# Optimization experiments

Measured on AMD Instinct MI355X. Metric: run time of the kernel, lower is better.

## Reference

```python
import jax, jax.numpy as jnp
import numpy as np

B, N, CIN = 4, 8192, 256
H, D = 8, 64            # n_heads, head_n_channels
INNER = H * D           # 512
COUT = 256
EPS = 1e-5              # torch InstanceNorm1d default eps


def setup_inputs() -> dict:
    key = jax.random.key(0)
    ks = jax.random.split(key, 8)
    s = 1.0 / np.sqrt(CIN)
    return {
        "u_x": jax.random.normal(ks[0], (B, N, CIN), dtype=jnp.float32),
        "pos_x": jax.random.uniform(ks[1], (B, N, 2), dtype=jnp.float32),
        # torch nn.Linear weights have shape (out_features, in_features)
        "Wq": jax.random.normal(ks[2], (INNER, CIN), dtype=jnp.float32) * s,
        "Wk": jax.random.normal(ks[3], (INNER, CIN), dtype=jnp.float32) * s,
        "Wv": jax.random.normal(ks[4], (INNER, CIN), dtype=jnp.float32) * s,
        "Wo": jax.random.normal(ks[5], (COUT, INNER), dtype=jnp.float32) * (1.0 / np.sqrt(INNER)),
        "bo": jax.random.normal(ks[6], (COUT,), dtype=jnp.float32) * 0.01,
    }


def _heads(x, W):
    # x: [B,N,CIN] @ W.T -> [B,N,H*D] -> [B,H,N,D]
    y = jnp.einsum("bnc,ec->bne", x, W)
    return y.reshape(x.shape[0], x.shape[1], H, D).transpose(0, 2, 1, 3)


def _inorm(u):
    # Matches torch: InstanceNorm1d applied to (B*H, N, D) normalizes over the
    # LAST dim (D) per (batch, head, grid point), biased variance, no affine.
    mean = jnp.mean(u, axis=-1, keepdims=True)
    var = jnp.mean(jnp.square(u - mean), axis=-1, keepdims=True)
    return (u - mean) / jnp.sqrt(var + EPS)


def reference(u_x, pos_x, Wq, Wk, Wv, Wo, bo):
    batch, n = u_x.shape[0], u_x.shape[1]
    q = _heads(u_x, Wq)          # [B,H,N,D]
    k = _inorm(_heads(u_x, Wk))  # u_y = u_x (self-attention path)
    v = _inorm(_heads(u_x, Wv))
    # associative path: (K^T V) then Q; uniform weights = 1/N
    dots = jnp.einsum("bhnd,bhne->bhde", k, v)   # [B,H,D,D]
    u = jnp.einsum("bhnd,bhde->bhne", q, dots) / n
    u = u.transpose(0, 2, 1, 3).reshape(batch, n, INNER)
    return jnp.einsum("bne,oe->bno", u, Wo) + bo
```

## Files before the change

kernel.cpp:

```cpp
#include <hip/hip_runtime.h>


#define B_    4
#define N_    8192
#define CIN_  256
#define H_    8
#define D_    64
#define INNER_ 512
#define COUT_ 256
#define EPS_  1e-5f

typedef unsigned short ushort_t;
typedef unsigned int   uint_t;
typedef __attribute__((ext_vector_type(8))) short short8;
typedef __attribute__((ext_vector_type(4))) float f32x4;

__device__ __forceinline__ void split_bf16(float x, ushort_t& hi, ushort_t& lo) {
  const uint_t u = __float_as_uint(x);
  const uint_t hr = (u + 0x8000u) & 0xffff0000u;
  hi = (ushort_t)(hr >> 16);
  const float l = x - __uint_as_float(hr);
  lo = (ushort_t)((__float_as_uint(l) + 0x8000u) >> 16);
}

__device__ __forceinline__ void cvt8(float4 x, float4 y, uint4& uh, uint4& ul) {
  const float v[8] = {x.x, x.y, x.z, x.w, y.x, y.y, y.z, y.w};
  ushort_t h[8], l[8];
#pragma unroll
  for (int j = 0; j < 8; j++) split_bf16(v[j], h[j], l[j]);
  uh = make_uint4(h[0] | ((uint_t)h[1] << 16), h[2] | ((uint_t)h[3] << 16),
                  h[4] | ((uint_t)h[5] << 16), h[6] | ((uint_t)h[7] << 16));
  ul = make_uint4(l[0] | ((uint_t)l[1] << 16), l[2] | ((uint_t)l[3] << 16),
                  l[4] | ((uint_t)l[5] << 16), l[6] | ((uint_t)l[7] << 16));
}

#define MFMA(A, Bv, C) __builtin_amdgcn_mfma_f32_16x16x32_bf16((A), (Bv), (C), 0, 0, 0)

__global__ __launch_bounds__(256) void prep_all_kernel(
    const float* __restrict__ u_x, const float* __restrict__ Wk,
    const float* __restrict__ Wv, ushort_t* __restrict__ uxH,
    ushort_t* __restrict__ uxL, ushort_t* __restrict__ WkvH,
    ushort_t* __restrict__ WkvL, float* __restrict__ dots)
{
  const int bid = blockIdx.x;
  if (bid < 4096) {
    const size_t base = ((size_t)bid * 256 + threadIdx.x) * 8;
    const float4 x = *(const float4*)(u_x + base);
    const float4 y = *(const float4*)(u_x + base + 4);
    uint4 uh, ul;
    cvt8(x, y, uh, ul);
    *(uint4*)(uxH + base) = uh;
    *(uint4*)(uxL + base) = ul;
  } else {
    const int wb = bid - 4096;
    const size_t base = ((size_t)wb * 256 + threadIdx.x) * 8;
    const float* src = (base < 131072) ? (Wk + base) : (Wv + base - 131072);
    const float4 x = *(const float4*)(src);
    const float4 y = *(const float4*)(src + 4);
    uint4 uh, ul;
    cvt8(x, y, uh, ul);
    *(uint4*)(WkvH + base) = uh;
    *(uint4*)(WkvL + base) = ul;
    *(float4*)(dots + ((size_t)wb * 256 + threadIdx.x) * 4) =
        make_float4(0.f, 0.f, 0.f, 0.f);
  }
}

__global__ __launch_bounds__(256, 2) void kv_dots_kernel(
    const ushort_t* __restrict__ uxH, const ushort_t* __restrict__ uxL,
    const ushort_t* __restrict__ WkvH, const ushort_t* __restrict__ WkvL,
    float* __restrict__ dots)
{
  __shared__ __align__(16) char smem[66560];
  ushort_t* KtH = (ushort_t*)(smem);
  ushort_t* KtL = (ushort_t*)(smem + 9216);
  ushort_t* VtH = (ushort_t*)(smem + 18432);
  ushort_t* VtL = (ushort_t*)(smem + 27648);

  const int t = threadIdx.x;
  const int chunk = blockIdx.x, h = blockIdx.y, b = blockIdx.z;
  const int lane = t & 63, wave = t >> 6;
  const int q = lane >> 4, r = lane & 15;
  const int m0 = (wave >> 1) * 64, n0 = (wave & 1) * 64;
  const int srow = t >> 1, scs = (t & 1) * 16, q0 = (t & 1) * 2;
  const int dstripe = 16 * wave;

  const int wr = (srow < 64) ? (h * 64 + srow) : (512 + h * 64 + srow - 64);
  const ushort_t* bgH = WkvH + (size_t)wr * CIN_ + scs;
  const ushort_t* bgL = WkvL + (size_t)wr * CIN_ + scs;

  f32x4 dacc[4];
#pragma unroll
  for (int j = 0; j < 4; j++) dacc[j] = (f32x4)0.f;

  for (int mt = 0; mt < 2; mt++) {
    const int r0 = chunk * 256 + mt * 128;
    const ushort_t* agH = uxH + ((size_t)(b * N_) + r0 + srow) * CIN_ + scs;
    const ushort_t* agL = uxL + ((size_t)(b * N_) + r0 + srow) * CIN_ + scs;

    f32x4 acc[4][4];
#pragma unroll
    for (int i = 0; i < 4; i++)
#pragma unroll
      for (int j = 0; j < 4; j++) acc[i][j] = (f32x4)0.f;

    {
      const uint4 a0 = *(const uint4*)(agH);
      const uint4 a1 = *(const uint4*)(agH + 8);
      const uint4 l0 = *(const uint4*)(agL);
      const uint4 l1 = *(const uint4*)(agL + 8);
      const uint4 b0 = *(const uint4*)(bgH);
      const uint4 b1 = *(const uint4*)(bgH + 8);
      const uint4 c0 = *(const uint4*)(bgL);
      const uint4 c1 = *(const uint4*)(bgL + 8);
      ushort_t (*Ah)[130][8] = (ushort_t(*)[130][8])(smem);
      ushort_t (*Al)[130][8] = (ushort_t(*)[130][8])(smem + 8320);
      ushort_t (*Bh)[130][8] = (ushort_t(*)[130][8])(smem + 16640);
      ushort_t (*Bl)[130][8] = (ushort_t(*)[130][8])(smem + 24960);
      *(uint4*)&Ah[q0][srow][0] = a0;  *(uint4*)&Ah[q0 + 1][srow][0] = a1;
      *(uint4*)&Al[q0][srow][0] = l0;  *(uint4*)&Al[q0 + 1][srow][0] = l1;
      *(uint4*)&Bh[q0][srow][0] = b0;  *(uint4*)&Bh[q0 + 1][srow][0] = b1;
      *(uint4*)&Bl[q0][srow][0] = c0;  *(uint4*)&Bl[q0 + 1][srow][0] = c1;
    }
    __syncthreads();

#pragma unroll 2
    for (int kc = 0; kc < 8; kc++) {
      const int cur = kc & 1, nxt = cur ^ 1;
      uint4 a0, a1, l0, l1, b0, b1, c0, c1;
      if (kc < 7) {
        const int off = (kc + 1) * 32;
        a0 = *(const uint4*)(agH + off);  a1 = *(const uint4*)(agH + off + 8);
        l0 = *(const uint4*)(agL + off);  l1 = *(const uint4*)(agL + off + 8);
        b0 = *(const uint4*)(bgH + off);  b1 = *(const uint4*)(bgH + off + 8);
        c0 = *(const uint4*)(bgL + off);  c1 = *(const uint4*)(bgL + off + 8);
      }
      char* sc = smem + cur * 33280;
      ushort_t (*Ah)[130][8] = (ushort_t(*)[130][8])(sc);
      ushort_t (*Al)[130][8] = (ushort_t(*)[130][8])(sc + 8320);
      ushort_t (*Bh)[130][8] = (ushort_t(*)[130][8])(sc + 16640);
      ushort_t (*Bl)[130][8] = (ushort_t(*)[130][8])(sc + 24960);
      short8 ahf[4], alf[4];
#pragma unroll
      for (int mi = 0; mi < 4; mi++) {
        ahf[mi] = *(const short8*)&Ah[q][m0 + 16 * mi + r][0];
        alf[mi] = *(const short8*)&Al[q][m0 + 16 * mi + r][0];
      }
#pragma unroll
      for (int nj = 0; nj < 4; nj++) {
        const short8 bhv = *(const short8*)&Bh[q][n0 + 16 * nj + r][0];
        const short8 blv = *(const short8*)&Bl[q][n0 + 16 * nj + r][0];
#pragma unroll
        for (int mi = 0; mi < 4; mi++) {
          acc[mi][nj] = MFMA(ahf[mi], bhv, acc[mi][nj]);
          acc[mi][nj] = MFMA(alf[mi], bhv, acc[mi][nj]);
          acc[mi][nj] = MFMA(ahf[mi], blv, acc[mi][nj]);
        }
      }
      if (kc < 7) {
        char* sn = smem + nxt * 33280;
        ushort_t (*nAh)[130][8] = (ushort_t(*)[130][8])(sn);
        ushort_t (*nAl)[130][8] = (ushort_t(*)[130][8])(sn + 8320);
        ushort_t (*nBh)[130][8] = (ushort_t(*)[130][8])(sn + 16640);
        ushort_t (*nBl)[130][8] = (ushort_t(*)[130][8])(sn + 24960);
        *(uint4*)&nAh[q0][srow][0] = a0;  *(uint4*)&nAh[q0 + 1][srow][0] = a1;
        *(uint4*)&nAl[q0][srow][0] = l0;  *(uint4*)&nAl[q0 + 1][srow][0] = l1;
        *(uint4*)&nBh[q0][srow][0] = b0;  *(uint4*)&nBh[q0 + 1][srow][0] = b1;
        *(uint4*)&nBl[q0][srow][0] = c0;  *(uint4*)&nBl[q0 + 1][srow][0] = c1;
      }
      __syncthreads();
    }

    float mean[4][4], inv[4][4];
#pragma unroll
    for (int mi = 0; mi < 4; mi++)
#pragma unroll
      for (int reg = 0; reg < 4; reg++) {
        float rs = 0.f, rq = 0.f;
#pragma unroll
        for (int nj = 0; nj < 4; nj++) {
          const float v = acc[mi][nj][reg];
          rs += v;
          rq = fmaf(v, v, rq);
        }
#pragma unroll
        for (int msk = 1; msk < 16; msk <<= 1) {
          rs += __shfl_xor(rs, msk, 64);
          rq += __shfl_xor(rq, msk, 64);
        }
        const float m = rs * (1.f / 64.f);
        const float var = fmaxf(rq * (1.f / 64.f) - m * m, 0.f);
        mean[mi][reg] = m;
        inv[mi][reg] = rsqrtf(var + EPS_);
      }
#pragma unroll
    for (int mi = 0; mi < 4; mi++)
#pragma unroll
      for (int nj = 0; nj < 4; nj++)
#pragma unroll
        for (int reg = 0; reg < 4; reg++)
          acc[mi][nj][reg] = (acc[mi][nj][reg] - mean[mi][reg]) * inv[mi][reg];

    for (int p = 0; p < 2; p++) {
      if ((wave >> 1) == p) {
        ushort_t* Hd = (wave & 1) ? VtH : KtH;
        ushort_t* Ld = (wave & 1) ? VtL : KtL;
#pragma unroll
        for (int nj = 0; nj < 4; nj++) {
          const int d = 16 * nj + r;
#pragma unroll
          for (int mi = 0; mi < 4; mi++) {
            const int nb = 16 * mi + 4 * q;
            ushort_t hh[4], ll[4];
#pragma unroll
            for (int reg = 0; reg < 4; reg++)
              split_bf16(acc[mi][nj][reg], hh[reg], ll[reg]);
            uint2 ph, pl;
            ph.x = hh[0] | ((uint_t)hh[1] << 16);
            ph.y = hh[2] | ((uint_t)hh[3] << 16);
            pl.x = ll[0] | ((uint_t)ll[1] << 16);
            pl.y = ll[2] | ((uint_t)ll[3] << 16);
            *(uint2*)&Hd[d * 72 + nb] = ph;
            *(uint2*)&Ld[d * 72 + nb] = pl;
          }
        }
      }
      __syncthreads();
#pragma unroll
      for (int ks = 0; ks < 2; ks++) {
        const short8 aH = *(const short8*)&KtH[(dstripe + r) * 72 + ks * 32 + q * 8];
        const short8 aL = *(const short8*)&KtL[(dstripe + r) * 72 + ks * 32 + q * 8];
#pragma unroll
        for (int ej = 0; ej < 4; ej++) {
          const short8 bH = *(const short8*)&VtH[(16 * ej + r) * 72 + ks * 32 + q * 8];
          const short8 bL = *(const short8*)&VtL[(16 * ej + r) * 72 + ks * 32 + q * 8];
          dacc[ej] = MFMA(aH, bH, dacc[ej]);
          dacc[ej] = MFMA(aL, bH, dacc[ej]);
          dacc[ej] = MFMA(aH, bL, dacc[ej]);
        }
      }
      __syncthreads();
    }
  }

  float* dg = dots + ((size_t)(b * H_ + h)) * 4096;
#pragma unroll
  for (int ej = 0; ej < 4; ej++)
#pragma unroll
    for (int reg = 0; reg < 4; reg++)
      atomicAdd(&dg[(dstripe + 4 * q + reg) * 64 + 16 * ej + r], dacc[ej][reg]);
}

__global__ __launch_bounds__(256) void s_kernel(
    const float* __restrict__ dots, const float* __restrict__ Wo,
    float* __restrict__ S)
{
  const int blk = blockIdx.x;
  const int b = blk >> 9, hd = blk & 511, h = hd >> 6;
  __shared__ float drow[64];
  const int t = threadIdx.x;
  if (t < 64) drow[t] = dots[((size_t)(b * H_ + h)) * 4096 + (hd & 63) * 64 + t];
  __syncthreads();
  const float* wp = Wo + (size_t)t * INNER_ + h * 64;
  float acc = 0.f;
#pragma unroll
  for (int e = 0; e < 64; e += 4) {
    const float4 w = *(const float4*)(wp + e);
    acc = fmaf(drow[e + 0], w.x, acc);
    acc = fmaf(drow[e + 1], w.y, acc);
    acc = fmaf(drow[e + 2], w.z, acc);
    acc = fmaf(drow[e + 3], w.w, acc);
  }
  S[((size_t)(b * INNER_) + hd) * COUT_ + t] = acc;
}

__global__ __launch_bounds__(256) void mb_part_kernel(
    const float* __restrict__ Wq, const float* __restrict__ S,
    float* __restrict__ Mbp)
{
  __shared__ __align__(16) float wql[128][16];
  const int c0 = blockIdx.x * 16, b = blockIdx.y, s = blockIdx.z;
  const int t = threadIdx.x;
#pragma unroll
  for (int i = 0; i < 8; i++) {
    const int idx = i * 256 + t;
    wql[idx >> 4][idx & 15] = Wq[(size_t)(s * 128 + (idx >> 4)) * CIN_ + c0 + (idx & 15)];
  }
  __syncthreads();
  float acc[16];
#pragma unroll
  for (int cp = 0; cp < 16; cp++) acc[cp] = 0.f;
  const float* sp = S + ((size_t)(b * INNER_) + s * 128) * COUT_ + t;
  for (int hd = 0; hd < 128; hd++) {
    const float sv = sp[(size_t)hd * COUT_];
#pragma unroll
    for (int g = 0; g < 4; g++) {
      const float4 w = *(const float4*)&wql[hd][g * 4];
      acc[g * 4 + 0] = fmaf(w.x, sv, acc[g * 4 + 0]);
      acc[g * 4 + 1] = fmaf(w.y, sv, acc[g * 4 + 1]);
      acc[g * 4 + 2] = fmaf(w.z, sv, acc[g * 4 + 2]);
      acc[g * 4 + 3] = fmaf(w.w, sv, acc[g * 4 + 3]);
    }
  }
#pragma unroll
  for (int cp = 0; cp < 16; cp++)
    Mbp[(((size_t)s * 4 + b) * CIN_ + c0 + cp) * COUT_ + t] = acc[cp];
}

__global__ __launch_bounds__(256) void mb_merge_kernel(
    const float* __restrict__ Mbp, ushort_t* __restrict__ MbtH,
    ushort_t* __restrict__ MbtL)
{
  const int c0 = blockIdx.x * 16, b = blockIdx.y;
  const int o = threadIdx.x;
#pragma unroll
  for (int cp = 0; cp < 16; cp++) {
    const int c = c0 + cp;
    float v = 0.f;
#pragma unroll
    for (int s = 0; s < 4; s++)
      v += Mbp[(((size_t)s * 4 + b) * CIN_ + c) * COUT_ + o];
    v *= (1.0f / N_);
    ushort_t hi, lo;
    split_bf16(v, hi, lo);
    const size_t off = ((size_t)(b * COUT_) + o) * CIN_ + c;
    MbtH[off] = hi;
    MbtL[off] = lo;
  }
}

__global__ __launch_bounds__(256, 4) void out_kernel(
    const ushort_t* __restrict__ uxH, const ushort_t* __restrict__ uxL,
    const ushort_t* __restrict__ MbtH, const ushort_t* __restrict__ MbtL,
    const float* __restrict__ bo, float* __restrict__ out)
{
  __shared__ __align__(16) char smem[33280];
  ushort_t (*Ah)[130][8] = (ushort_t(*)[130][8])(smem);
  ushort_t (*Al)[130][8] = (ushort_t(*)[130][8])(smem + 8320);
  ushort_t (*Bh)[130][8] = (ushort_t(*)[130][8])(smem + 16640);
  ushort_t (*Bl)[130][8] = (ushort_t(*)[130][8])(smem + 24960);

  const int t = threadIdx.x;
  const int r0 = blockIdx.x * 128, o0 = blockIdx.y * 128, b = blockIdx.z;
  const int lane = t & 63, wave = t >> 6;
  const int q = lane >> 4, r = lane & 15;
  const int m0 = (wave >> 1) * 64, n0 = (wave & 1) * 64;
  const int srow = t >> 1, scs = (t & 1) * 16, q0 = (t & 1) * 2;

  const ushort_t* agH = uxH + ((size_t)(b * N_) + r0 + srow) * CIN_ + scs;
  const ushort_t* agL = uxL + ((size_t)(b * N_) + r0 + srow) * CIN_ + scs;
  const ushort_t* bgH = MbtH + ((size_t)(b * COUT_) + o0 + srow) * CIN_ + scs;
  const ushort_t* bgL = MbtL + ((size_t)(b * COUT_) + o0 + srow) * CIN_ + scs;

  f32x4 acc[4][4];
#pragma unroll
  for (int i = 0; i < 4; i++)
#pragma unroll
    for (int j = 0; j < 4; j++) acc[i][j] = (f32x4)0.f;

  for (int kc = 0; kc < 8; kc++) {
    *(uint4*)&Ah[q0][srow][0]     = *(const uint4*)(agH + kc * 32);
    *(uint4*)&Ah[q0 + 1][srow][0] = *(const uint4*)(agH + kc * 32 + 8);
    *(uint4*)&Al[q0][srow][0]     = *(const uint4*)(agL + kc * 32);
    *(uint4*)&Al[q0 + 1][srow][0] = *(const uint4*)(agL + kc * 32 + 8);
    *(uint4*)&Bh[q0][srow][0]     = *(const uint4*)(bgH + kc * 32);
    *(uint4*)&Bh[q0 + 1][srow][0] = *(const uint4*)(bgH + kc * 32 + 8);
    *(uint4*)&Bl[q0][srow][0]     = *(const uint4*)(bgL + kc * 32);
    *(uint4*)&Bl[q0 + 1][srow][0] = *(const uint4*)(bgL + kc * 32 + 8);
    __syncthreads();
    short8 ahf[4], alf[4];
#pragma unroll
    for (int mi = 0; mi < 4; mi++) {
      ahf[mi] = *(const short8*)&Ah[q][m0 + 16 * mi + r][0];
      alf[mi] = *(const short8*)&Al[q][m0 + 16 * mi + r][0];
    }
#pragma unroll
    for (int nj = 0; nj < 4; nj++) {
      const short8 bhv = *(const short8*)&Bh[q][n0 + 16 * nj + r][0];
      const short8 blv = *(const short8*)&Bl[q][n0 + 16 * nj + r][0];
#pragma unroll
      for (int mi = 0; mi < 4; mi++) {
        acc[mi][nj] = MFMA(ahf[mi], bhv, acc[mi][nj]);
        acc[mi][nj] = MFMA(alf[mi], bhv, acc[mi][nj]);
        acc[mi][nj] = MFMA(ahf[mi], blv, acc[mi][nj]);
      }
    }
    __syncthreads();
  }

  float bov[4];
#pragma unroll
  for (int nj = 0; nj < 4; nj++) bov[nj] = bo[o0 + n0 + 16 * nj + r];
#pragma unroll
  for (int mi = 0; mi < 4; mi++)
#pragma unroll
    for (int nj = 0; nj < 4; nj++) {
      const f32x4 v = acc[mi][nj];
#pragma unroll
      for (int reg = 0; reg < 4; reg++) {
        const int row = r0 + m0 + 16 * mi + q * 4 + reg;
        out[((size_t)(b * N_) + row) * COUT_ + o0 + n0 + 16 * nj + r] =
            v[reg] + bov[nj];
      }
    }
}

extern "C" void kernel_launch(void* const* d_in, const int* in_sizes, int n_in,
                              void* d_out, int out_size, void* d_ws, size_t ws_size,
                              hipStream_t stream) {
  const float* u_x = (const float*)d_in[0];
  const float* Wq = (const float*)d_in[2];
  const float* Wk = (const float*)d_in[3];
  const float* Wv = (const float*)d_in[4];
  const float* Wo = (const float*)d_in[5];
  const float* bo = (const float*)d_in[6];
  float* out = (float*)d_out;

  ushort_t* uxH  = (ushort_t*)d_ws;
  ushort_t* uxL  = uxH + 8388608;
  ushort_t* WkvH = uxL + 8388608;
  ushort_t* WkvL = WkvH + 262144;
  ushort_t* MbtH = WkvL + 262144;
  ushort_t* MbtL = MbtH + 262144;
  float* dots = (float*)(MbtL + 262144);
  float* S    = dots + 131072;
  float* Mbp  = S + 524288;

  prep_all_kernel<<<4224, 256, 0, stream>>>(u_x, Wk, Wv, uxH, uxL, WkvH, WkvL, dots);
  kv_dots_kernel<<<dim3(32, 8, 4), 256, 0, stream>>>(uxH, uxL, WkvH, WkvL, dots);
  s_kernel<<<2048, 256, 0, stream>>>(dots, Wo, S);
  mb_part_kernel<<<dim3(16, 4, 4), 256, 0, stream>>>(Wq, S, Mbp);
  mb_merge_kernel<<<dim3(16, 4), 256, 0, stream>>>(Mbp, MbtH, MbtL);
  out_kernel<<<dim3(64, 2, 4), 256, 0, stream>>>(uxH, uxL, MbtH, MbtL, bo, out);
}
```

Baseline: 231.0 us.

## Fuse S/Mb small-matrix kernels into one and widen K/V dots staging tile

```diff
diff --git a/kernel.cpp b/kernel.cpp
--- a/kernel.cpp
+++ b/kernel.cpp
@@ -71,11 +71,11 @@
     const ushort_t* __restrict__ WkvH, const ushort_t* __restrict__ WkvL,
     float* __restrict__ dots)
 {
-  __shared__ __align__(16) char smem[66560];
+  __shared__ __align__(16) char smem[69632];
   ushort_t* KtH = (ushort_t*)(smem);
-  ushort_t* KtL = (ushort_t*)(smem + 9216);
-  ushort_t* VtH = (ushort_t*)(smem + 18432);
-  ushort_t* VtL = (ushort_t*)(smem + 27648);
+  ushort_t* KtL = (ushort_t*)(smem + 17408);
+  ushort_t* VtH = (ushort_t*)(smem + 34816);
+  ushort_t* VtL = (ushort_t*)(smem + 52224);
 
   const int t = threadIdx.x;
   const int chunk = blockIdx.x, h = blockIdx.y, b = blockIdx.z;
@@ -193,54 +193,48 @@
         mean[mi][reg] = m;
         inv[mi][reg] = rsqrtf(var + EPS_);
       }
-#pragma unroll
-    for (int mi = 0; mi < 4; mi++)
-#pragma unroll
-      for (int nj = 0; nj < 4; nj++)
-#pragma unroll
-        for (int reg = 0; reg < 4; reg++)
-          acc[mi][nj][reg] = (acc[mi][nj][reg] - mean[mi][reg]) * inv[mi][reg];
-
-    for (int p = 0; p < 2; p++) {
-      if ((wave >> 1) == p) {
-        ushort_t* Hd = (wave & 1) ? VtH : KtH;
-        ushort_t* Ld = (wave & 1) ? VtL : KtL;
-#pragma unroll
-        for (int nj = 0; nj < 4; nj++) {
-          const int d = 16 * nj + r;
-#pragma unroll
-          for (int mi = 0; mi < 4; mi++) {
-            const int nb = 16 * mi + 4 * q;
-            ushort_t hh[4], ll[4];
-#pragma unroll
-            for (int reg = 0; reg < 4; reg++)
-              split_bf16(acc[mi][nj][reg], hh[reg], ll[reg]);
-            uint2 ph, pl;
-            ph.x = hh[0] | ((uint_t)hh[1] << 16);
-            ph.y = hh[2] | ((uint_t)hh[3] << 16);
-            pl.x = ll[0] | ((uint_t)ll[1] << 16);
-            pl.y = ll[2] | ((uint_t)ll[3] << 16);
-            *(uint2*)&Hd[d * 72 + nb] = ph;
-            *(uint2*)&Ld[d * 72 + nb] = pl;
+
+    {
+      ushort_t* DH = (wave & 1) ? VtH : KtH;
+      ushort_t* DL = (wave & 1) ? VtL : KtL;
+#pragma unroll
+      for (int nj = 0; nj < 4; nj++) {
+        const int d = 16 * nj + r;
+#pragma unroll
+        for (int mi = 0; mi < 4; mi++) {
+          const int cc = m0 + 16 * mi + 4 * q;
+          ushort_t hh[4], ll[4];
+#pragma unroll
+          for (int reg = 0; reg < 4; reg++) {
+            const float v = (acc[mi][nj][reg] - mean[mi][reg]) * inv[mi][reg];
+            split_bf16(v, hh[reg], ll[reg]);
           }
+          uint2 ph, pl;
+          ph.x = hh[0] | ((uint_t)hh[1] << 16);
+          ph.y = hh[2] | ((uint_t)hh[3] << 16);
+          pl.x = ll[0] | ((uint_t)ll[1] << 16);
+          pl.y = ll[2] | ((uint_t)ll[3] << 16);
+          *(uint2*)&DH[d * 136 + cc] = ph;
+          *(uint2*)&DL[d * 136 + cc] = pl;
         }
       }
-      __syncthreads();
-#pragma unroll
-      for (int ks = 0; ks < 2; ks++) {
-        const short8 aH = *(const short8*)&KtH[(dstripe + r) * 72 + ks * 32 + q * 8];
-        const short8 aL = *(const short8*)&KtL[(dstripe + r) * 72 + ks * 32 + q * 8];
-#pragma unroll
-        for (int ej = 0; ej < 4; ej++) {
-          const short8 bH = *(const short8*)&VtH[(16 * ej + r) * 72 + ks * 32 + q * 8];
-          const short8 bL = *(const short8*)&VtL[(16 * ej + r) * 72 + ks * 32 + q * 8];
-          dacc[ej] = MFMA(aH, bH, dacc[ej]);
-          dacc[ej] = MFMA(aL, bH, dacc[ej]);
-          dacc[ej] = MFMA(aH, bL, dacc[ej]);
-        }
-      }
-      __syncthreads();
-    }
+    }
+    __syncthreads();
+
+#pragma unroll
+    for (int ks = 0; ks < 4; ks++) {
+      const short8 aH = *(const short8*)&KtH[(dstripe + r) * 136 + ks * 32 + q * 8];
+      const short8 aL = *(const short8*)&KtL[(dstripe + r) * 136 + ks * 32 + q * 8];
+#pragma unroll
+      for (int ej = 0; ej < 4; ej++) {
+        const short8 bH = *(const short8*)&VtH[(16 * ej + r) * 136 + ks * 32 + q * 8];
+        const short8 bL = *(const short8*)&VtL[(16 * ej + r) * 136 + ks * 32 + q * 8];
+        dacc[ej] = MFMA(aH, bH, dacc[ej]);
+        dacc[ej] = MFMA(aL, bH, dacc[ej]);
+        dacc[ej] = MFMA(aH, bL, dacc[ej]);
+      }
+    }
+    __syncthreads();
   }
 
   float* dg = dots + ((size_t)(b * H_ + h)) * 4096;
@@ -251,79 +245,55 @@
       atomicAdd(&dg[(dstripe + 4 * q + reg) * 64 + 16 * ej + r], dacc[ej][reg]);
 }
 
-__global__ __launch_bounds__(256) void s_kernel(
+__global__ __launch_bounds__(256) void mid_kernel(
     const float* __restrict__ dots, const float* __restrict__ Wo,
-    float* __restrict__ S)
-{
-  const int blk = blockIdx.x;
-  const int b = blk >> 9, hd = blk & 511, h = hd >> 6;
-  __shared__ float drow[64];
-  const int t = threadIdx.x;
-  if (t < 64) drow[t] = dots[((size_t)(b * H_ + h)) * 4096 + (hd & 63) * 64 + t];
-  __syncthreads();
-  const float* wp = Wo + (size_t)t * INNER_ + h * 64;
-  float acc = 0.f;
-#pragma unroll
-  for (int e = 0; e < 64; e += 4) {
-    const float4 w = *(const float4*)(wp + e);
-    acc = fmaf(drow[e + 0], w.x, acc);
-    acc = fmaf(drow[e + 1], w.y, acc);
-    acc = fmaf(drow[e + 2], w.z, acc);
-    acc = fmaf(drow[e + 3], w.w, acc);
-  }
-  S[((size_t)(b * INNER_) + hd) * COUT_ + t] = acc;
-}
-
-__global__ __launch_bounds__(256) void mb_part_kernel(
-    const float* __restrict__ Wq, const float* __restrict__ S,
-    float* __restrict__ Mbp)
-{
-  __shared__ __align__(16) float wql[128][16];
-  const int c0 = blockIdx.x * 16, b = blockIdx.y, s = blockIdx.z;
-  const int t = threadIdx.x;
-#pragma unroll
-  for (int i = 0; i < 8; i++) {
-    const int idx = i * 256 + t;
-    wql[idx >> 4][idx & 15] = Wq[(size_t)(s * 128 + (idx >> 4)) * CIN_ + c0 + (idx & 15)];
-  }
-  __syncthreads();
-  float acc[16];
-#pragma unroll
-  for (int cp = 0; cp < 16; cp++) acc[cp] = 0.f;
-  const float* sp = S + ((size_t)(b * INNER_) + s * 128) * COUT_ + t;
-  for (int hd = 0; hd < 128; hd++) {
-    const float sv = sp[(size_t)hd * COUT_];
-#pragma unroll
-    for (int g = 0; g < 4; g++) {
-      const float4 w = *(const float4*)&wql[hd][g * 4];
-      acc[g * 4 + 0] = fmaf(w.x, sv, acc[g * 4 + 0]);
-      acc[g * 4 + 1] = fmaf(w.y, sv, acc[g * 4 + 1]);
-      acc[g * 4 + 2] = fmaf(w.z, sv, acc[g * 4 + 2]);
-      acc[g * 4 + 3] = fmaf(w.w, sv, acc[g * 4 + 3]);
-    }
-  }
-#pragma unroll
-  for (int cp = 0; cp < 16; cp++)
-    Mbp[(((size_t)s * 4 + b) * CIN_ + c0 + cp) * COUT_ + t] = acc[cp];
-}
-
-__global__ __launch_bounds__(256) void mb_merge_kernel(
-    const float* __restrict__ Mbp, ushort_t* __restrict__ MbtH,
+    const float* __restrict__ Wq, ushort_t* __restrict__ MbtH,
     ushort_t* __restrict__ MbtL)
 {
-  const int c0 = blockIdx.x * 16, b = blockIdx.y;
-  const int o = threadIdx.x;
-#pragma unroll
-  for (int cp = 0; cp < 16; cp++) {
-    const int c = c0 + cp;
-    float v = 0.f;
-#pragma unroll
-    for (int s = 0; s < 4; s++)
-      v += Mbp[(((size_t)s * 4 + b) * CIN_ + c) * COUT_ + o];
-    v *= (1.0f / N_);
+  __shared__ float WoL[8][520];
+  __shared__ float S_loc[512][9];
+  const int o0 = blockIdx.x * 8, b = blockIdx.y;
+  const int t = threadIdx.x;
+
+#pragma unroll
+  for (int i = 0; i < 16; i++) {
+    const int idx = i * 256 + t;
+    WoL[idx >> 9][idx & 511] = Wo[(size_t)(o0 + (idx >> 9)) * INNER_ + (idx & 511)];
+  }
+  __syncthreads();
+
+#pragma unroll
+  for (int hh = 0; hh < 2; hh++) {
+    const int hd = hh * 256 + t, h = hd >> 6, d = hd & 63;
+    const float* dr = dots + ((size_t)(b * H_ + h)) * 4096 + d * 64;
+    float row[64];
+#pragma unroll
+    for (int e = 0; e < 64; e += 4) *(float4*)&row[e] = *(const float4*)(dr + e);
+#pragma unroll
+    for (int o = 0; o < 8; o++) {
+      float s = 0.f;
+#pragma unroll
+      for (int e = 0; e < 64; e++) s = fmaf(row[e], WoL[o][h * 64 + e], s);
+      S_loc[hd][o] = s;
+    }
+  }
+  __syncthreads();
+
+  float acc[8];
+#pragma unroll
+  for (int o = 0; o < 8; o++) acc[o] = 0.f;
+#pragma unroll 8
+  for (int hd = 0; hd < INNER_; hd++) {
+    const float w = Wq[(size_t)hd * CIN_ + t];
+#pragma unroll
+    for (int o = 0; o < 8; o++) acc[o] = fmaf(w, S_loc[hd][o], acc[o]);
+  }
+#pragma unroll
+  for (int o = 0; o < 8; o++) {
+    const float v = acc[o] * (1.0f / N_);
     ushort_t hi, lo;
     split_bf16(v, hi, lo);
-    const size_t off = ((size_t)(b * COUT_) + o) * CIN_ + c;
+    const size_t off = ((size_t)(b * COUT_) + o0 + o) * CIN_ + t;
     MbtH[off] = hi;
     MbtL[off] = lo;
   }
@@ -423,13 +393,9 @@
   ushort_t* MbtH = WkvL + 262144;
   ushort_t* MbtL = MbtH + 262144;
   float* dots = (float*)(MbtL + 262144);
-  float* S    = dots + 131072;
-  float* Mbp  = S + 524288;
 
   prep_all_kernel<<<4224, 256, 0, stream>>>(u_x, Wk, Wv, uxH, uxL, WkvH, WkvL, dots);
   kv_dots_kernel<<<dim3(32, 8, 4), 256, 0, stream>>>(uxH, uxL, WkvH, WkvL, dots);
-  s_kernel<<<2048, 256, 0, stream>>>(dots, Wo, S);
-  mb_part_kernel<<<dim3(16, 4, 4), 256, 0, stream>>>(Wq, S, Mbp);
-  mb_merge_kernel<<<dim3(16, 4), 256, 0, stream>>>(Mbp, MbtH, MbtL);
+  mid_kernel<<<dim3(32, 4), 256, 0, stream>>>(dots, Wo, Wq, MbtH, MbtL);
   out_kernel<<<dim3(64, 2, 4), 256, 0, stream>>>(uxH, uxL, MbtH, MbtL, bo, out);
 }
```

Result: no change. 231.1 us (+0.0%).
